# Kernel tuning notes

Measured on AMD Instinct MI355X. Metric: run time of the kernel, lower is better.

## Reference

```python
import jax, jax.numpy as jnp
import numpy as np

N = 100_000      # total nodes across batch of graphs
E = 1_600_000    # total directed edges
D = 128          # input feature dim
H = 128          # hidden dim
OUT = 10         # output classes
B = 500          # number of graphs (200 nodes each)
L_MID = 3        # GIN layers after the first (num_layers-2)


def setup_inputs() -> dict:
    key = jax.random.key(0)
    ks = jax.random.split(key, 24)
    s = np.float32(1.0 / np.sqrt(H))
    f32 = jnp.float32
    inp = {
        'node_features': jax.random.normal(ks[0], (N, D), f32),
        'edge_src': jax.random.randint(ks[1], (E,), 0, N, jnp.int32),
        'edge_dst': jax.random.randint(ks[2], (E,), 0, N, jnp.int32),
        'graph_ids': (jnp.arange(N) // (N // B)).astype(jnp.int32),
        # GIN eps per layer (torch init: zeros)
        'eps': jnp.zeros((4,), f32),
        # pre MLP (input layer): Linear(D,H) -> BN -> ReLU -> Linear(H,H), then pre_batchnorm
        'pre_W1': jax.random.normal(ks[3], (D, H), f32) * s,
        'pre_b1': jnp.zeros((H,), f32),
        'pre_g1': jnp.ones((H,), f32),
        'pre_bt1': jnp.zeros((H,), f32),
        'pre_W2': jax.random.normal(ks[4], (H, H), f32) * s,
        'pre_b2': jnp.zeros((H,), f32),
        'pre_gout': jnp.ones((H,), f32),
        'pre_btout': jnp.zeros((H,), f32),
        # middle GIN layers (stacked over L_MID)
        'mlp_W1': jax.random.normal(ks[5], (L_MID, H, H), f32) * s,
        'mlp_b1': jnp.zeros((L_MID, H), f32),
        'mlp_g1': jnp.ones((L_MID, H), f32),
        'mlp_bt1': jnp.zeros((L_MID, H), f32),
        'mlp_W2': jax.random.normal(ks[6], (L_MID, H, H), f32) * s,
        'mlp_b2': jnp.zeros((L_MID, H), f32),
        'bn_g': jnp.ones((L_MID, H), f32),
        'bn_bt': jnp.zeros((L_MID, H), f32),
        # per-layer prediction heads
        'pred_W0': jax.random.normal(ks[7], (D, OUT), f32) * s,
        'pred_b0': jnp.zeros((OUT,), f32),
        'pred_W': jax.random.normal(ks[8], (4, H, OUT), f32) * s,
        'pred_b': jnp.zeros((4, OUT), f32),
    }
    return inp


def _mlp_bn(x, W1, b1, g1, bt1, W2, b2, go, bo):
    # MLP(num_mlp_layers=2): Linear -> BN(eval) -> ReLU -> Linear, then outer BN(eval) -> ReLU
    h = jax.nn.relu(g1 * (x @ W1 + b1) + bt1)
    h = h @ W2 + b2
    return jax.nn.relu(go * h + bo)


def reference(node_features, edge_src, edge_dst, graph_ids, eps,
              pre_W1, pre_b1, pre_g1, pre_bt1, pre_W2, pre_b2, pre_gout, pre_btout,
              mlp_W1, mlp_b1, mlp_g1, mlp_bt1, mlp_W2, mlp_b2, bn_g, bn_bt,
              pred_W0, pred_b0, pred_W, pred_b):
    def agg(h):
        # sparse Adj @ h via gather + segment_sum (sum neighbor pooling, learn_eps=True -> no self loops)
        return jax.ops.segment_sum(h[edge_src], edge_dst, num_segments=N)

    h = node_features
    reps = [h]
    pooled = agg(h) + (1.0 + eps[0]) * h
    h = _mlp_bn(pooled, pre_W1, pre_b1, pre_g1, pre_bt1, pre_W2, pre_b2, pre_gout, pre_btout)
    reps.append(h)
    for i in range(L_MID):
        pooled = agg(h) + (1.0 + eps[i + 1]) * h
        h = _mlp_bn(pooled, mlp_W1[i], mlp_b1[i], mlp_g1[i], mlp_bt1[i],
                    mlp_W2[i], mlp_b2[i], bn_g[i], bn_bt[i])
        reps.append(h)

    # graph-level sum pooling + per-layer linear heads (dropout off in eval)
    score = jax.ops.segment_sum(reps[0], graph_ids, num_segments=B) @ pred_W0 + pred_b0
    for k in range(4):
        score = score + jax.ops.segment_sum(reps[k + 1], graph_ids, num_segments=B) @ pred_W[k] + pred_b[k]
    return score  # [B, OUT]
```

## Files before the change

### kernel.cpp

```cpp
#include <hip/hip_runtime.h>
#include <hip/hip_bf16.h>

#define NN 100000
#define EE 1600000
#define HH 128
#define OUTC 10
#define BB 500
#define GSZ 200
#define LDA 136

#define NBKT 782
#define BCAP 2560
#define EPB 4096
#define NBUCKB 391
#define NTILE64 1563

typedef float f32x4 __attribute__((ext_vector_type(4)));
typedef __bf16 bf16x8 __attribute__((ext_vector_type(8)));

__device__ __forceinline__ float b2f(unsigned short u){
    unsigned int x = ((unsigned int)u) << 16;
    return __builtin_bit_cast(float, x);
}
__device__ __forceinline__ unsigned short f2b(float f){
    __hip_bfloat16 h = __float2bfloat16(f);
    return __builtin_bit_cast(unsigned short, h);
}

__global__ __launch_bounds__(256) void k_setup(const int* __restrict__ src, const int* __restrict__ dst,
                                               int* __restrict__ bucket_cursor, unsigned int* __restrict__ ebuf,
                                               const float* __restrict__ x, unsigned short* __restrict__ hA,
                                               float* __restrict__ G,
                                               const float* __restrict__ preW1, const float* __restrict__ preW2,
                                               const float* __restrict__ mlpW1, const float* __restrict__ mlpW2,
                                               unsigned short* __restrict__ Wbf){
    __shared__ __align__(16) unsigned int sval[EPB];
    __shared__ unsigned short sbkt[EPB];
    __shared__ int shist[NBKT];
    int t = threadIdx.x;
    int bid = blockIdx.x;

    if (bid < NBUCKB){
        int e0 = bid * EPB;
        for (int i = t; i < NBKT; i += 256) shist[i] = 0;
        __syncthreads();
        for (int i = t; i < EPB; i += 256){
            int e = e0 + i;
            if (e < EE){
                int d = dst[e];
                int b = d >> 7;
                sval[i] = ((unsigned)src[e] << 7) | (unsigned)(d & 127);
                sbkt[i] = (unsigned short)b;
                atomicAdd(&shist[b], 1);
            } else {
                sbkt[i] = 0xffff;
            }
        }
        __syncthreads();
        for (int i = t; i < NBKT; i += 256){
            int c = shist[i];
            shist[i] = c ? atomicAdd(&bucket_cursor[i], c) : 0;
        }
        __syncthreads();
        for (int i = t; i < EPB; i += 256){
            unsigned short b = sbkt[i];
            if (b != 0xffff){
                int pos = atomicAdd(&shist[b], 1);
                if (pos < BCAP) ebuf[(int)b * BCAP + pos] = sval[i];
            }
        }
    } else if (bid < NBUCKB + BB){
        float* r0 = (float*)sval;
        float* r1 = r0 + 256;
        int g = bid - NBUCKB;
        int f2 = t & 63;
        int rg = t >> 6;
        if (t < 128){
            #pragma unroll
            for (int k = 1; k < 5; ++k) G[(size_t)k*BB*128 + g*128 + t] = 0.f;
        }
        float a0 = 0.f, a1 = 0.f;
        for (int i = rg; i < GSZ; i += 4){
            int node = g*GSZ + i;
            float2 v = *(const float2*)(x + (size_t)node*128 + f2*2);
            a0 += v.x; a1 += v.y;
            unsigned int o = (unsigned)f2b(v.x) | ((unsigned)f2b(v.y) << 16);
            ((unsigned int*)hA)[(size_t)node*64 + f2] = o;
        }
        r0[t] = a0; r1[t] = a1;
        __syncthreads();
        if (t < 64){
            float s0 = r0[t] + r0[t+64] + r0[t+128] + r0[t+192];
            float s1 = r1[t] + r1[t+64] + r1[t+128] + r1[t+192];
            float2 v; v.x = s0; v.y = s1;
            *(float2*)(G + g*128 + t*2) = v;
        }
    } else {
        int idx = (bid - NBUCKB - BB)*256 + t;
        int w = idx >> 14;
        int rem = idx & 16383;
        int e = rem & 7;
        int chunk = rem >> 3;
        int m = chunk & 15;
        int q = (chunk >> 4) & 3;
        int kk = (chunk >> 6) & 3;
        int j = chunk >> 8;
        int n = j*16 + m;
        int k = kk*32 + q*8 + e;
        const float* s;
        if      (w == 0) s = preW1;
        else if (w == 1) s = preW2;
        else if (w <  5) s = mlpW1 + (w-2)*16384;
        else             s = mlpW2 + (w-5)*16384;
        Wbf[idx] = f2b(s[k*128 + n]);
    }
}

__global__ __launch_bounds__(1024) void k_bscan(const int* __restrict__ bucket_cursor,
                                                int* __restrict__ bucket_base, int* __restrict__ row_ptr){
    __shared__ int tmp[1024];
    int t = threadIdx.x;
    int v = (t < NBKT) ? min(bucket_cursor[t], BCAP) : 0;
    tmp[t] = v; __syncthreads();
    for (int off = 1; off < 1024; off <<= 1){
        int a = (t >= off) ? tmp[t - off] : 0;
        __syncthreads();
        tmp[t] += a;
        __syncthreads();
    }
    if (t < NBKT) bucket_base[t + 1] = tmp[t];
    if (t == 0){ bucket_base[0] = 0; row_ptr[NN] = EE; }
}

__global__ __launch_bounds__(256) void k_csr(const int* __restrict__ bucket_cursor, const int* __restrict__ bucket_base,
                                             const unsigned int* __restrict__ ebuf,
                                             int* __restrict__ row_ptr, int* __restrict__ col){
    __shared__ int cnt[128];
    __shared__ int pfx[128];
    int b = blockIdx.x;
    int t = threadIdx.x;
    int c    = min(bucket_cursor[b], BCAP);
    int base = bucket_base[b];
    if (t < 128) cnt[t] = 0;
    __syncthreads();
    const unsigned int* eb = ebuf + (size_t)b * BCAP;
    for (int i = t; i < c; i += 256) atomicAdd(&cnt[eb[i] & 127], 1);
    __syncthreads();
    if (t == 0){
        int run = 0;
        for (int i = 0; i < 128; ++i){ pfx[i] = run; run += cnt[i]; }
    }
    __syncthreads();
    int node0 = b * 128;
    if (t < 128 && node0 + t < NN) row_ptr[node0 + t] = base + pfx[t];
    if (t < 128) cnt[t] = pfx[t];
    __syncthreads();
    for (int i = t; i < c; i += 256){
        unsigned int v = eb[i];
        int pos = atomicAdd(&cnt[v & 127], 1);
        col[base + pos] = (int)(v >> 7);
    }
}

__device__ __forceinline__ void acc_u32(float* a, unsigned int v, int j){
    a[j]   += __builtin_bit_cast(float, v << 16);
    a[j+1] += __builtin_bit_cast(float, v & 0xffff0000u);
}
__device__ __forceinline__ void acc_u4(float* a, uint4 v){
    acc_u32(a, v.x, 0); acc_u32(a, v.y, 2); acc_u32(a, v.z, 4); acc_u32(a, v.w, 6);
}
__device__ __forceinline__ uint4 and4(uint4 v, unsigned mk){
    v.x &= mk; v.y &= mk; v.z &= mk; v.w &= mk; return v;
}

__global__ __launch_bounds__(256) void k_agg(const int* __restrict__ row_ptr, const int* __restrict__ col,
                                             const unsigned short* __restrict__ h,
                                             const float* __restrict__ eps, int l,
                                             unsigned short* __restrict__ pooled){
    int lane = threadIdx.x & 63;
    int wv   = threadIdx.x >> 6;
    int n    = blockIdx.x*4 + wv;
    int q = lane >> 4;
    int u = lane & 15;
    int beg = row_ptr[n], end = row_ptr[n+1];
    float a[8];
    #pragma unroll
    for (int j = 0; j < 8; ++j) a[j] = 0.f;

    int e = beg;
    for (; e + 16 <= end; e += 16){
        int c0 = col[e      + q];
        int c1 = col[e + 4  + q];
        int c2 = col[e + 8  + q];
        int c3 = col[e + 12 + q];
        uint4 v0 = *(const uint4*)(h + (size_t)c0*128 + u*8);
        uint4 v1 = *(const uint4*)(h + (size_t)c1*128 + u*8);
        uint4 v2 = *(const uint4*)(h + (size_t)c2*128 + u*8);
        uint4 v3 = *(const uint4*)(h + (size_t)c3*128 + u*8);
        acc_u4(a, v0); acc_u4(a, v1); acc_u4(a, v2); acc_u4(a, v3);
    }
    if (e < end){
        int last = end - 1;
        int i0 = e + q, i1 = e + 4 + q, i2 = e + 8 + q, i3 = e + 12 + q;
        int c0 = col[min(i0, last)];
        int c1 = col[min(i1, last)];
        int c2 = col[min(i2, last)];
        int c3 = col[min(i3, last)];
        uint4 v0 = *(const uint4*)(h + (size_t)c0*128 + u*8);
        uint4 v1 = *(const uint4*)(h + (size_t)c1*128 + u*8);
        uint4 v2 = *(const uint4*)(h + (size_t)c2*128 + u*8);
        uint4 v3 = *(const uint4*)(h + (size_t)c3*128 + u*8);
        v0 = and4(v0, (i0 < end) ? 0xffffffffu : 0u);
        v1 = and4(v1, (i1 < end) ? 0xffffffffu : 0u);
        v2 = and4(v2, (i2 < end) ? 0xffffffffu : 0u);
        v3 = and4(v3, (i3 < end) ? 0xffffffffu : 0u);
        acc_u4(a, v0); acc_u4(a, v1); acc_u4(a, v2); acc_u4(a, v3);
    }
    #pragma unroll
    for (int j = 0; j < 8; ++j){
        a[j] += __shfl_xor(a[j], 16, 64);
        a[j] += __shfl_xor(a[j], 32, 64);
    }
    if (q == 0){
        float ep = 1.0f + eps[l];
        uint4 hs = *(const uint4*)(h + (size_t)n*128 + u*8);
        a[0] += ep * __builtin_bit_cast(float, hs.x << 16);
        a[1] += ep * __builtin_bit_cast(float, hs.x & 0xffff0000u);
        a[2] += ep * __builtin_bit_cast(float, hs.y << 16);
        a[3] += ep * __builtin_bit_cast(float, hs.y & 0xffff0000u);
        a[4] += ep * __builtin_bit_cast(float, hs.z << 16);
        a[5] += ep * __builtin_bit_cast(float, hs.z & 0xffff0000u);
        a[6] += ep * __builtin_bit_cast(float, hs.w << 16);
        a[7] += ep * __builtin_bit_cast(float, hs.w & 0xffff0000u);
        uint4 o;
        o.x = (unsigned)f2b(a[0]) | ((unsigned)f2b(a[1]) << 16);
        o.y = (unsigned)f2b(a[2]) | ((unsigned)f2b(a[3]) << 16);
        o.z = (unsigned)f2b(a[4]) | ((unsigned)f2b(a[5]) << 16);
        o.w = (unsigned)f2b(a[6]) | ((unsigned)f2b(a[7]) << 16);
        *(uint4*)(pooled + (size_t)n*128 + u*8) = o;
    }
}

__device__ __forceinline__ void load_a(const unsigned short* __restrict__ Ain, int tile,
                                       int wv, int m, int q, bf16x8* dst){
    int node = tile*64 + wv*16 + m;
    bool valid = node < NN;
    const unsigned short* base = Ain + (size_t)(valid ? node : 0)*128 + q*8;
    #pragma unroll
    for (int kk = 0; kk < 4; ++kk){
        int4 v = *(const int4*)(base + kk*32);
        if (!valid) v = make_int4(0,0,0,0);
        dst[kk] = __builtin_bit_cast(bf16x8, v);
    }
}

__global__ __launch_bounds__(256, 4) void k_mlp1(const unsigned short* __restrict__ Ain,
                                                 unsigned short* __restrict__ Yout,
                                                 const unsigned short* __restrict__ Wf,
                                                 const float* __restrict__ bb, const float* __restrict__ gg,
                                                 const float* __restrict__ bt){
    __shared__ __align__(16) unsigned short Wl[16384];
    __shared__ __align__(16) unsigned short Ys[4][16*LDA];
    int t = threadIdx.x;
    int lane = t & 63, wv = t >> 6;
    int m = lane & 15, q = lane >> 4;
    for (int i = t; i < 2048; i += 256)
        *(int4*)(&Wl[i*8]) = *(const int4*)(Wf + i*8);
    __syncthreads();
    float ge[8], ce[8];
    #pragma unroll
    for (int j = 0; j < 8; ++j){
        int colc = j*16 + m;
        float gv = gg[colc];
        ge[j] = gv; ce[j] = bb[colc]*gv + bt[colc];
    }
    unsigned short* Y = &Ys[wv][0];
    int tile = blockIdx.x;
    bf16x8 aN[4];
    if (tile < NTILE64) load_a(Ain, tile, wv, m, q, aN);
    while (tile < NTILE64){
        bf16x8 a[4];
        #pragma unroll
        for (int kk = 0; kk < 4; ++kk) a[kk] = aN[kk];
        int nxt = tile + gridDim.x;
        if (nxt < NTILE64) load_a(Ain, nxt, wv, m, q, aN);
        f32x4 acc[8];
        #pragma unroll
        for (int j = 0; j < 8; ++j) acc[j] = (f32x4){0.f,0.f,0.f,0.f};
        #pragma unroll
        for (int kk = 0; kk < 4; ++kk){
            #pragma unroll
            for (int j = 0; j < 8; ++j){
                bf16x8 b = *(const bf16x8*)(&Wl[((((j*4+kk)*4+q)*16)+m)*8]);
                acc[j] = __builtin_amdgcn_mfma_f32_16x16x32_bf16(a[kk], b, acc[j], 0, 0, 0);
            }
        }
        #pragma unroll
        for (int j = 0; j < 8; ++j){
            int colc = j*16 + m;
            #pragma unroll
            for (int r = 0; r < 4; ++r){
                float v = fmaxf(acc[j][r]*ge[j] + ce[j], 0.f);
                Y[(q*4 + r)*LDA + colc] = f2b(v);
            }
        }
        #pragma unroll
        for (int i = 0; i < 4; ++i){
            int idx = i*64 + lane;
            int r = idx >> 4, c = idx & 15;
            int nd = tile*64 + wv*16 + r;
            if (nd < NN)
                *(int4*)(Yout + (size_t)nd*128 + c*8) = *(const int4*)(&Y[r*LDA + c*8]);
        }
        tile = nxt;
    }
}

__global__ __launch_bounds__(256, 4) void k_mlp2(const unsigned short* __restrict__ Ain,
                                                 unsigned short* __restrict__ Out,
                                                 const unsigned short* __restrict__ Wf,
                                                 const float* __restrict__ bb, const float* __restrict__ gg,
                                                 const float* __restrict__ bt,
                                                 float* __restrict__ Gout){
    __shared__ __align__(16) unsigned short Wl[16384];
    __shared__ __align__(16) unsigned short Ys[4][16*LDA];
    int t = threadIdx.x;
    int lane = t & 63, wv = t >> 6;
    int m = lane & 15, q = lane >> 4;
    for (int i = t; i < 2048; i += 256)
        *(int4*)(&Wl[i*8]) = *(const int4*)(Wf + i*8);
    __syncthreads();
    float ge[8], ce[8];
    #pragma unroll
    for (int j = 0; j < 8; ++j){
        int colc = j*16 + m;
        float gv = gg[colc];
        ge[j] = gv; ce[j] = bb[colc]*gv + bt[colc];
    }
    unsigned short* Y = &Ys[wv][0];
    int tile = blockIdx.x;
    bf16x8 aN[4];
    if (tile < NTILE64) load_a(Ain, tile, wv, m, q, aN);
    while (tile < NTILE64){
        bf16x8 a[4];
        #pragma unroll
        for (int kk = 0; kk < 4; ++kk) a[kk] = aN[kk];
        int nxt = tile + gridDim.x;
        if (nxt < NTILE64) load_a(Ain, nxt, wv, m, q, aN);
        f32x4 acc[8];
        #pragma unroll
        for (int j = 0; j < 8; ++j) acc[j] = (f32x4){0.f,0.f,0.f,0.f};
        #pragma unroll
        for (int kk = 0; kk < 4; ++kk){
            #pragma unroll
            for (int j = 0; j < 8; ++j){
                bf16x8 b = *(const bf16x8*)(&Wl[((((j*4+kk)*4+q)*16)+m)*8]);
                acc[j] = __builtin_amdgcn_mfma_f32_16x16x32_bf16(a[kk], b, acc[j], 0, 0, 0);
            }
        }
        #pragma unroll
        for (int j = 0; j < 8; ++j){
            int colc = j*16 + m;
            #pragma unroll
            for (int r = 0; r < 4; ++r){
                float v = fmaxf(acc[j][r]*ge[j] + ce[j], 0.f);
                Y[(q*4 + r)*LDA + colc] = f2b(v);
            }
        }
        int row0 = tile*64 + wv*16;
        #pragma unroll
        for (int i = 0; i < 4; ++i){
            int idx = i*64 + lane;
            int r = idx >> 4, c = idx & 15;
            int nd = row0 + r;
            if (nd < NN)
                *(int4*)(Out + (size_t)nd*128 + c*8) = *(const int4*)(&Y[r*LDA + c*8]);
        }
        {
            float run0 = 0.f, run1 = 0.f;
            int curg = row0 / GSZ;
            for (int r = 0; r < 16; ++r){
                int nd = row0 + r;
                if (nd >= NN) break;
                int g = nd / GSZ;
                if (g != curg){
                    if (run0 != 0.f) atomicAdd(&Gout[curg*128 + lane*2], run0);
                    if (run1 != 0.f) atomicAdd(&Gout[curg*128 + lane*2 + 1], run1);
                    run0 = 0.f; run1 = 0.f; curg = g;
                }
                unsigned int v = *(const unsigned int*)(&Y[r*LDA + lane*2]);
                run0 += b2f((unsigned short)v);
                run1 += b2f((unsigned short)(v >> 16));
            }
            if (run0 != 0.f) atomicAdd(&Gout[curg*128 + lane*2], run0);
            if (run1 != 0.f) atomicAdd(&Gout[curg*128 + lane*2 + 1], run1);
        }
        tile = nxt;
    }
}

__global__ __launch_bounds__(256) void k_score(const float* __restrict__ G,
                                               const float* __restrict__ W0, const float* __restrict__ b0,
                                               const float* __restrict__ Wk, const float* __restrict__ bk,
                                               float* __restrict__ out){
    int id = blockIdx.x*256 + threadIdx.x;
    if (id >= BB*OUTC) return;
    int b = id / OUTC, o = id % OUTC;
    float s = b0[o];
    #pragma unroll
    for (int k = 0; k < 4; ++k) s += bk[k*OUTC + o];
    const float* g0 = G + b*128;
    for (int c = 0; c < 128; ++c) s += g0[c] * W0[c*OUTC + o];
    for (int k = 0; k < 4; ++k){
        const float* gk = G + (size_t)(k+1)*BB*128 + b*128;
        const float* wk = Wk + k*128*OUTC;
        for (int c = 0; c < 128; ++c) s += gk[c] * wk[c*OUTC + o];
    }
    out[id] = s;
}

extern "C" void kernel_launch(void* const* d_in, const int* in_sizes, int n_in,
                              void* d_out, int out_size, void* d_ws, size_t ws_size,
                              hipStream_t stream){
    const float* node_features = (const float*)d_in[0];
    const int*   edge_src  = (const int*)d_in[1];
    const int*   edge_dst  = (const int*)d_in[2];
    const float* eps       = (const float*)d_in[4];
    const float* pre_W1    = (const float*)d_in[5];
    const float* pre_b1    = (const float*)d_in[6];
    const float* pre_g1    = (const float*)d_in[7];
    const float* pre_bt1   = (const float*)d_in[8];
    const float* pre_W2    = (const float*)d_in[9];
    const float* pre_b2    = (const float*)d_in[10];
    const float* pre_gout  = (const float*)d_in[11];
    const float* pre_btout = (const float*)d_in[12];
    const float* mlp_W1    = (const float*)d_in[13];
    const float* mlp_b1    = (const float*)d_in[14];
    const float* mlp_g1    = (const float*)d_in[15];
    const float* mlp_bt1   = (const float*)d_in[16];
    const float* mlp_W2    = (const float*)d_in[17];
    const float* mlp_b2    = (const float*)d_in[18];
    const float* bn_g      = (const float*)d_in[19];
    const float* bn_bt     = (const float*)d_in[20];
    const float* pred_W0   = (const float*)d_in[21];
    const float* pred_b0   = (const float*)d_in[22];
    const float* pred_W    = (const float*)d_in[23];
    const float* pred_b    = (const float*)d_in[24];
    float* out = (float*)d_out;

    char* p = (char*)d_ws;
    auto alloc = [&](size_t bytes)->char*{
        char* r = p;
        p += (bytes + 255) & ~(size_t)255;
        return r;
    };
    int* bucket_cursor    = (int*)alloc((size_t)NBKT*4);
    int* bucket_base      = (int*)alloc((size_t)(NBKT+1)*4);
    int* row_ptr          = (int*)alloc((size_t)(NN+1)*4);
    int* col              = (int*)alloc((size_t)EE*4);
    unsigned int* ebuf    = (unsigned int*)alloc((size_t)NBKT*BCAP*4);
    unsigned short* Wbf   = (unsigned short*)alloc((size_t)8*128*128*2);
    unsigned short* hA    = (unsigned short*)alloc((size_t)NN*128*2);
    unsigned short* hB    = (unsigned short*)alloc((size_t)NN*128*2);
    unsigned short* pooled= (unsigned short*)alloc((size_t)NN*128*2);
    float* G              = (float*)alloc((size_t)5*BB*128*4);

    hipMemsetAsync(bucket_cursor, 0, (size_t)NBKT*4, stream);

    k_setup<<<NBUCKB + BB + 512, 256, 0, stream>>>(edge_src, edge_dst, bucket_cursor, ebuf,
                                                   node_features, hA, G,
                                                   pre_W1, pre_W2, mlp_W1, mlp_W2, Wbf);
    k_bscan<<<1, 1024, 0, stream>>>(bucket_cursor, bucket_base, row_ptr);
    k_csr<<<NBKT, 256, 0, stream>>>(bucket_cursor, bucket_base, ebuf, row_ptr, col);

    const unsigned short* hcur = hA;
    unsigned short* hnxt = hB;
    for (int l = 0; l < 4; ++l){
        k_agg<<<NN/4, 256, 0, stream>>>(row_ptr, col, hcur, eps, l, pooled);
        const unsigned short *W1t, *W2t;
        const float *b1,*g1,*bt1,*b2,*g2,*bt2;
        if (l == 0){
            W1t = Wbf;             W2t = Wbf + 16384;
            b1 = pre_b1; g1 = pre_g1; bt1 = pre_bt1;
            b2 = pre_b2; g2 = pre_gout; bt2 = pre_btout;
        } else {
            W1t = Wbf + (size_t)(2 + (l-1))*16384;
            W2t = Wbf + (size_t)(5 + (l-1))*16384;
            b1 = mlp_b1 + (l-1)*128; g1 = mlp_g1 + (l-1)*128; bt1 = mlp_bt1 + (l-1)*128;
            b2 = mlp_b2 + (l-1)*128; g2 = bn_g   + (l-1)*128; bt2 = bn_bt   + (l-1)*128;
        }
        k_mlp1<<<768, 256, 0, stream>>>(pooled, pooled, W1t, b1, g1, bt1);
        k_mlp2<<<768, 256, 0, stream>>>(pooled, hnxt, W2t, b2, g2, bt2,
                                        G + (size_t)(l+1)*BB*128);
        const unsigned short* tmp = hnxt;
        hnxt = (unsigned short*)hcur;
        hcur = tmp;
    }
    k_score<<<(BB*OUTC + 255)/256, 256, 0, stream>>>(G, pred_W0, pred_b0, pred_W, pred_b, out);
}
```

Before: 607.1 us.

## Fuse the two MLP GEMM kernels into one with the intermediate kept in LDS

Merges k_mlp1 and k_mlp2 into one kernel. Both weight matrices are loaded into shared memory, and the first GEMM's BN+ReLU output stays in the per-wave LDS tile, where it becomes the A operand of the second GEMM. This removes the global write and re-read of the hidden activations and one launch per layer. The block grows to 512 threads over 128-row tiles, launched as 256 blocks, and LDS use per block roughly doubles, which lowers occupancy.

```diff
diff --git a/kernel.cpp b/kernel.cpp
--- a/kernel.cpp
+++ b/kernel.cpp
@@ -13,7 +13,7 @@
 #define BCAP 2560
 #define EPB 4096
 #define NBUCKB 391
-#define NTILE64 1563
+#define NTILE128 782
 
 typedef float f32x4 __attribute__((ext_vector_type(4)));
 typedef __bf16 bf16x8 __attribute__((ext_vector_type(8)));
@@ -243,7 +243,7 @@
 
 __device__ __forceinline__ void load_a(const unsigned short* __restrict__ Ain, int tile,
                                        int wv, int m, int q, bf16x8* dst){
-    int node = tile*64 + wv*16 + m;
+    int node = tile*128 + wv*16 + m;
     bool valid = node < NN;
     const unsigned short* base = Ain + (size_t)(valid ? node : 0)*128 + q*8;
     #pragma unroll
@@ -254,36 +254,44 @@
     }
 }
 
-__global__ __launch_bounds__(256, 4) void k_mlp1(const unsigned short* __restrict__ Ain,
-                                                 unsigned short* __restrict__ Yout,
-                                                 const unsigned short* __restrict__ Wf,
-                                                 const float* __restrict__ bb, const float* __restrict__ gg,
-                                                 const float* __restrict__ bt){
-    __shared__ __align__(16) unsigned short Wl[16384];
-    __shared__ __align__(16) unsigned short Ys[4][16*LDA];
+__global__ __launch_bounds__(512, 2) void k_mlp(const unsigned short* __restrict__ Ain,
+                                                unsigned short* __restrict__ Out,
+                                                const unsigned short* __restrict__ Wf1,
+                                                const unsigned short* __restrict__ Wf2,
+                                                const float* __restrict__ b1v, const float* __restrict__ g1v,
+                                                const float* __restrict__ bt1v,
+                                                const float* __restrict__ b2v, const float* __restrict__ g2v,
+                                                const float* __restrict__ bt2v,
+                                                float* __restrict__ Gout){
+    __shared__ __align__(16) unsigned short W1l[16384];
+    __shared__ __align__(16) unsigned short W2l[16384];
+    __shared__ __align__(16) unsigned short Ys[8][16*LDA];
     int t = threadIdx.x;
     int lane = t & 63, wv = t >> 6;
     int m = lane & 15, q = lane >> 4;
-    for (int i = t; i < 2048; i += 256)
-        *(int4*)(&Wl[i*8]) = *(const int4*)(Wf + i*8);
+    #pragma unroll
+    for (int i = t; i < 2048; i += 512){
+        *(int4*)(&W1l[i*8]) = *(const int4*)(Wf1 + i*8);
+        *(int4*)(&W2l[i*8]) = *(const int4*)(Wf2 + i*8);
+    }
     __syncthreads();
-    float ge[8], ce[8];
+    float ge1[8], ce1[8], ge2[8], ce2[8];
     #pragma unroll
     for (int j = 0; j < 8; ++j){
         int colc = j*16 + m;
-        float gv = gg[colc];
-        ge[j] = gv; ce[j] = bb[colc]*gv + bt[colc];
+        float gv1 = g1v[colc]; ge1[j] = gv1; ce1[j] = b1v[colc]*gv1 + bt1v[colc];
+        float gv2 = g2v[colc]; ge2[j] = gv2; ce2[j] = b2v[colc]*gv2 + bt2v[colc];
     }
     unsigned short* Y = &Ys[wv][0];
     int tile = blockIdx.x;
     bf16x8 aN[4];
-    if (tile < NTILE64) load_a(Ain, tile, wv, m, q, aN);
-    while (tile < NTILE64){
+    if (tile < NTILE128) load_a(Ain, tile, wv, m, q, aN);
+    while (tile < NTILE128){
         bf16x8 a[4];
         #pragma unroll
         for (int kk = 0; kk < 4; ++kk) a[kk] = aN[kk];
         int nxt = tile + gridDim.x;
-        if (nxt < NTILE64) load_a(Ain, nxt, wv, m, q, aN);
+        if (nxt < NTILE128) load_a(Ain, nxt, wv, m, q, aN);
         f32x4 acc[8];
         #pragma unroll
         for (int j = 0; j < 8; ++j) acc[j] = (f32x4){0.f,0.f,0.f,0.f};
@@ -291,7 +299,7 @@
         for (int kk = 0; kk < 4; ++kk){
             #pragma unroll
             for (int j = 0; j < 8; ++j){
-                bf16x8 b = *(const bf16x8*)(&Wl[((((j*4+kk)*4+q)*16)+m)*8]);
+                bf16x8 b = *(const bf16x8*)(&W1l[((((j*4+kk)*4+q)*16)+m)*8]);
                 acc[j] = __builtin_amdgcn_mfma_f32_16x16x32_bf16(a[kk], b, acc[j], 0, 0, 0);
             }
         }
@@ -300,62 +308,20 @@
             int colc = j*16 + m;
             #pragma unroll
             for (int r = 0; r < 4; ++r){
-                float v = fmaxf(acc[j][r]*ge[j] + ce[j], 0.f);
+                float v = fmaxf(acc[j][r]*ge1[j] + ce1[j], 0.f);
                 Y[(q*4 + r)*LDA + colc] = f2b(v);
             }
         }
-        #pragma unroll
-        for (int i = 0; i < 4; ++i){
-            int idx = i*64 + lane;
-            int r = idx >> 4, c = idx & 15;
-            int nd = tile*64 + wv*16 + r;
-            if (nd < NN)
-                *(int4*)(Yout + (size_t)nd*128 + c*8) = *(const int4*)(&Y[r*LDA + c*8]);
-        }
-        tile = nxt;
-    }
-}
-
-__global__ __launch_bounds__(256, 4) void k_mlp2(const unsigned short* __restrict__ Ain,
-                                                 unsigned short* __restrict__ Out,
-                                                 const unsigned short* __restrict__ Wf,
-                                                 const float* __restrict__ bb, const float* __restrict__ gg,
-                                                 const float* __restrict__ bt,
-                                                 float* __restrict__ Gout){
-    __shared__ __align__(16) unsigned short Wl[16384];
-    __shared__ __align__(16) unsigned short Ys[4][16*LDA];
-    int t = threadIdx.x;
-    int lane = t & 63, wv = t >> 6;
-    int m = lane & 15, q = lane >> 4;
-    for (int i = t; i < 2048; i += 256)
-        *(int4*)(&Wl[i*8]) = *(const int4*)(Wf + i*8);
-    __syncthreads();
-    float ge[8], ce[8];
-    #pragma unroll
-    for (int j = 0; j < 8; ++j){
-        int colc = j*16 + m;
-        float gv = gg[colc];
-        ge[j] = gv; ce[j] = bb[colc]*gv + bt[colc];
-    }
-    unsigned short* Y = &Ys[wv][0];
-    int tile = blockIdx.x;
-    bf16x8 aN[4];
-    if (tile < NTILE64) load_a(Ain, tile, wv, m, q, aN);
-    while (tile < NTILE64){
-        bf16x8 a[4];
-        #pragma unroll
-        for (int kk = 0; kk < 4; ++kk) a[kk] = aN[kk];
-        int nxt = tile + gridDim.x;
-        if (nxt < NTILE64) load_a(Ain, nxt, wv, m, q, aN);
-        f32x4 acc[8];
-        #pragma unroll
-        for (int j = 0; j < 8; ++j) acc[j] = (f32x4){0.f,0.f,0.f,0.f};
+        f32x4 acc2[8];
+        #pragma unroll
+        for (int j = 0; j < 8; ++j) acc2[j] = (f32x4){0.f,0.f,0.f,0.f};
         #pragma unroll
         for (int kk = 0; kk < 4; ++kk){
+            bf16x8 ya = *(const bf16x8*)(&Y[m*LDA + kk*32 + q*8]);
             #pragma unroll
             for (int j = 0; j < 8; ++j){
-                bf16x8 b = *(const bf16x8*)(&Wl[((((j*4+kk)*4+q)*16)+m)*8]);
-                acc[j] = __builtin_amdgcn_mfma_f32_16x16x32_bf16(a[kk], b, acc[j], 0, 0, 0);
+                bf16x8 b = *(const bf16x8*)(&W2l[((((j*4+kk)*4+q)*16)+m)*8]);
+                acc2[j] = __builtin_amdgcn_mfma_f32_16x16x32_bf16(ya, b, acc2[j], 0, 0, 0);
             }
         }
         #pragma unroll
@@ -363,11 +329,11 @@
             int colc = j*16 + m;
             #pragma unroll
             for (int r = 0; r < 4; ++r){
-                float v = fmaxf(acc[j][r]*ge[j] + ce[j], 0.f);
+                float v = fmaxf(acc2[j][r]*ge2[j] + ce2[j], 0.f);
                 Y[(q*4 + r)*LDA + colc] = f2b(v);
             }
         }
-        int row0 = tile*64 + wv*16;
+        int row0 = tile*128 + wv*16;
         #pragma unroll
         for (int i = 0; i < 4; ++i){
             int idx = i*64 + lane;
@@ -489,9 +455,9 @@
             b1 = mlp_b1 + (l-1)*128; g1 = mlp_g1 + (l-1)*128; bt1 = mlp_bt1 + (l-1)*128;
             b2 = mlp_b2 + (l-1)*128; g2 = bn_g   + (l-1)*128; bt2 = bn_bt   + (l-1)*128;
         }
-        k_mlp1<<<768, 256, 0, stream>>>(pooled, pooled, W1t, b1, g1, bt1);
-        k_mlp2<<<768, 256, 0, stream>>>(pooled, hnxt, W2t, b2, g2, bt2,
-                                        G + (size_t)(l+1)*BB*128);
+        k_mlp<<<256, 512, 0, stream>>>(pooled, hnxt, W1t, W2t,
+                                       b1, g1, bt1, b2, g2, bt2,
+                                       G + (size_t)(l+1)*BB*128);
         const unsigned short* tmp = hnxt;
         hnxt = (unsigned short*)hcur;
         hcur = tmp;
```

Result: faster. 558.3 us (-8.0%).
